# Optimization experiments

Measured on AMD Instinct MI355X. Metric: run time of the kernel, lower is better.

The kernel has to match this reference:

```python
import jax, jax.numpy as jnp
import numpy as np

B, N, ND_, FEAT, WV = 32, 1024, 8, 2048, 300
E, T, STEPS = 20000, 2, 5
NDIM = N * ND_  # 8192


def setup_inputs() -> dict:
    key = jax.random.key(0)
    ks = jax.random.split(key, 20)
    s = 0.02
    inputs = jax.random.normal(ks[0], (B, FEAT), jnp.float32)
    wordvecs = jax.random.normal(ks[1], (N, WV), jnp.float32)
    # unique edges per type (disjoint across types) so the scatter has no duplicate indices
    rng = np.random.default_rng(0)
    codes = rng.permutation(N * N)[: T * E].reshape(T, E)
    edge_u = (codes // N).astype(np.int32)
    edge_v = (codes % N).astype(np.int32)
    ki = np.repeat(np.arange(ND_), ND_)
    kj = np.tile(np.arange(ND_), ND_)
    mat_u = (edge_u.reshape(-1)[:, None] * ND_ + ki[None, :]).reshape(-1).astype(np.int32)
    mat_v = (edge_v.reshape(-1)[:, None] * ND_ + kj[None, :]).reshape(-1).astype(np.int32)
    p = {
        'inputs': inputs, 'wordvecs': wordvecs,
        'edge_u': jnp.asarray(edge_u), 'edge_v': jnp.asarray(edge_v),
        'mat_u': jnp.asarray(mat_u), 'mat_v': jnp.asarray(mat_v),
        # Inputnet: Linear(feat+wv -> 512), Linear(512 -> node_dim)
        'W_in1': jax.random.normal(ks[2], (512, FEAT + WV), jnp.float32) * s,
        'b_in1': jnp.zeros((512,), jnp.float32),
        'W_in2': jax.random.normal(ks[3], (ND_, 512), jnp.float32) * s,
        'b_in2': jnp.zeros((ND_,), jnp.float32),
        # embnet: Linear(wv -> 50)
        'W_emb': jax.random.normal(ks[4], (50, WV), jnp.float32) * s,
        'b_emb': jnp.zeros((50,), jnp.float32),
        # relnets: one (50, 50*nd^2) matrix per edge type
        'rel_mats': jax.random.normal(ks[5], (T, 50, 50 * ND_ * ND_), jnp.float32) * s,
        # GRUCell(node_dim, node_dim)
        'W_ih': jax.random.normal(ks[6], (3 * ND_, ND_), jnp.float32) * s,
        'W_hh': jax.random.normal(ks[7], (3 * ND_, ND_), jnp.float32) * s,
        'b_ih': jnp.zeros((3 * ND_,), jnp.float32),
        'b_hh': jnp.zeros((3 * ND_,), jnp.float32),
        # outnet: Linear(nd -> 20), ReLU, Linear(20 -> 1)
        'W_o1': jax.random.normal(ks[8], (20, ND_), jnp.float32) * s,
        'b_o1': jnp.zeros((20,), jnp.float32),
        'W_o2': jax.random.normal(ks[9], (1, 20), jnp.float32) * s,
        'b_o2': jnp.zeros((1,), jnp.float32),
    }
    return p


def reference(inputs, wordvecs, edge_u, edge_v, mat_u, mat_v,
              W_in1, b_in1, W_in2, b_in2, W_emb, b_emb, rel_mats,
              W_ih, W_hh, b_ih, b_hh, W_o1, b_o1, W_o2, b_o2):
    nd = W_in2.shape[0]
    n_nodes = wordvecs.shape[0]
    ndim = n_nodes * nd
    bsz = inputs.shape[0]

    # Inputnet: per-(image, node) feature -> initial hidden state [B, N*nd]
    f = jnp.concatenate([
        jnp.broadcast_to(inputs[:, None, :], (bsz, n_nodes, inputs.shape[1])),
        jnp.broadcast_to(wordvecs[None, :, :], (bsz, n_nodes, wordvecs.shape[1])),
    ], axis=-1).reshape(bsz * n_nodes, -1)
    h = jax.nn.relu(f @ W_in1.T + b_in1) @ W_in2.T + b_in2  # [B*N, nd]
    hidden = h.reshape(bsz, ndim)

    # edge weights via Relnet per edge type
    embs = wordvecs @ W_emb.T + b_emb  # [N, 50]
    ws = []
    for t in range(rel_mats.shape[0]):
        ue = embs[edge_u[t]]  # [E, 50]
        ve = embs[edge_v[t]]  # [E, 50]
        tmp = (ue @ rel_mats[t]).reshape(ue.shape[0], embs.shape[1], nd * nd)
        ws.append(jnp.einsum('ed,edk->ek', ve, tmp))  # [E, nd^2]
    weights = jnp.concatenate(ws, axis=0).reshape(-1)

    # scatter into dense propagation matrix
    P = jnp.zeros((ndim, ndim), jnp.float32).at[mat_u, mat_v].set(weights)
    norm = jnp.sqrt(jnp.sum(P * P, axis=1))  # row L2 norms [ndim]
    norm = norm + (norm == 0).astype(P.dtype)
    P = P / norm  # NOTE: torch broadcasting divides COLUMNS by row norms (faithful)

    def gru(x, hc):
        gi = x @ W_ih.T + b_ih
        gh = hc @ W_hh.T + b_hh
        ir, iz, inn = jnp.split(gi, 3, axis=-1)
        hr, hz, hn = jnp.split(gh, 3, axis=-1)
        r = jax.nn.sigmoid(ir + hr)
        z = jax.nn.sigmoid(iz + hz)
        n = jnp.tanh(inn + r * hn)
        return (1.0 - z) * n + z * hc

    hiddens = [hidden]
    for _ in range(STEPS):
        x = jnp.tanh(hidden @ P.T)  # [B, ndim]
        hidden = gru(x.reshape(-1, nd), hidden.reshape(-1, nd)).reshape(bsz, ndim)
        hiddens.append(hidden)
    states = jnp.stack(hiddens, axis=1)  # [B, STEPS+1, ndim]

    o = jax.nn.relu(states.reshape(-1, nd) @ W_o1.T + b_o1) @ W_o2.T + b_o2  # [B*(S+1)*N, 1]
    logits = o.reshape(bsz, STEPS + 1, n_nodes).transpose(0, 2, 1)  # [B, N, S+1]
    return logits
```

## Files before the change

### kernel.cpp

```cpp
#include <hip/hip_runtime.h>
#include <math.h>

constexpr int B = 32, N = 1024, ND = 8, FEAT = 2048, WVD = 300;
constexpr int E = 20000, T = 2, STEPS = 5;
constexpr int NDIM = N * ND;
constexpr int H1 = 512;
constexpr int W1C = FEAT + WVD;
constexpr int EMB = 50;
constexpr int RC = EMB * ND * ND;
constexpr int KH = 150;
constexpr int CAP = 64;
constexpr int EQ = E / 4;

constexpr int G_KA   = 512;
constexpr int G_W1T  = 16 * 10;
constexpr int G_EMB  = N * 25 / 4;
constexpr int F1_TOT = G_KA + G_W1T + G_EMB;

constexpr int G_ARED = 8;
constexpr int G_WV   = 512;
constexpr int G_AHAT = 13 * 32 * T;
constexpr int F2_TOT = G_ARED + G_WV + G_AHAT;

__global__ __launch_bounds__(256) void k_f1(
        const float* inp, const float* W1, float* partA, float* W1T,
        const float* wv, const float* We, const float* be,
        float* embs, float* embsT) {
    __shared__ float smem[8 * 260];
    int tid = threadIdx.x;
    int blk = blockIdx.x;
    if (blk < G_KA) {
        int c = tid & 7, b = tid >> 3;
        int c0 = (blk & 63) * 8;
        int ks = blk >> 6;
        int kt = ks * 256;
        {
            int r = tid >> 5, cb = (tid & 31) * 8;
            const float* src = W1 + (size_t)(c0 + r) * W1C + kt + cb;
            float4 a0 = *(const float4*)src;
            float4 a1 = *(const float4*)(src + 4);
            *(float4*)&smem[r * 260 + cb] = a0;
            *(float4*)&smem[r * 260 + cb + 4] = a1;
        }
        __syncthreads();
        const float* xr = inp + (size_t)b * FEAT + kt;
        float acc = 0.f;
#pragma unroll 8
        for (int k4 = 0; k4 < 64; k4++) {
            float4 x = *(const float4*)(xr + k4 * 4);
            float4 w = *(const float4*)&smem[c * 260 + k4 * 4];
            acc += x.x * w.x + x.y * w.y + x.z * w.z + x.w * w.w;
        }
        partA[(size_t)ks * (H1 * B) + (c0 + c) * B + b] = acc;
    } else if (blk < G_KA + G_W1T) {
        int lb = blk - G_KA;
        int c0 = (lb % 16) * 32, k0 = (lb / 16) * 32;
        float (*tile)[33] = (float(*)[33])smem;
        int kl = tid & 31, cl4 = tid >> 5;
#pragma unroll
        for (int p = 0; p < 4; p++) {
            int c = cl4 + p * 8;
            int k = k0 + kl;
            if (k < WVD) tile[c][kl] = W1[(size_t)(c0 + c) * W1C + FEAT + k];
        }
        __syncthreads();
        int cl = tid & 31, kl4 = tid >> 5;
#pragma unroll
        for (int p = 0; p < 4; p++) {
            int kk = kl4 + p * 8;
            int k = k0 + kk;
            if (k < WVD) W1T[(size_t)k * H1 + c0 + cl] = tile[cl][kk];
        }
    } else {
        int lb = blk - G_KA - G_W1T;
        int wid = lb * 4 + (tid >> 6);
        int lane = tid & 63;
        int n = wid / 25, cp = wid - n * 25;
        int c0 = cp * 2;
        const float* xr = wv + (size_t)n * WVD;
        const float* wr0 = We + (size_t)c0 * WVD;
        const float* wr1 = wr0 + WVD;
        float a0 = 0.f, a1 = 0.f;
#pragma unroll
        for (int i = 0; i < 5; i++) {
            int k = i * 64 + lane;
            if (k < WVD) {
                float x = xr[k];
                a0 += x * wr0[k];
                a1 += x * wr1[k];
            }
        }
        for (int m = 32; m; m >>= 1) {
            a0 += __shfl_xor(a0, m, 64);
            a1 += __shfl_xor(a1, m, 64);
        }
        if (lane == 0) {
            float v0 = a0 + be[c0], v1 = a1 + be[c0 + 1];
            embs[n * EMB + c0] = v0;
            embs[n * EMB + c0 + 1] = v1;
            embsT[c0 * N + n] = v0;
            embsT[(c0 + 1) * N + n] = v1;
        }
    }
}

__global__ __launch_bounds__(256) void k_f2(
        const float* partA, float* AbT,
        const float* wv, const float* W1T, float* Wp,
        const float* embsT, const float* RMbase, float* Ahat) {
    __shared__ float smemf[1800];
    int tid = threadIdx.x, blk = blockIdx.x;
    if (blk < G_ARED) {
        int cb = blk * 2048 + tid * 8;
        float4 s0 = {0, 0, 0, 0}, s1 = {0, 0, 0, 0};
#pragma unroll
        for (int ks = 0; ks < 8; ks++) {
            const float* p = partA + (size_t)ks * (H1 * B) + cb;
            float4 a = *(const float4*)p;
            float4 b4 = *(const float4*)(p + 4);
            s0.x += a.x; s0.y += a.y; s0.z += a.z; s0.w += a.w;
            s1.x += b4.x; s1.y += b4.y; s1.z += b4.z; s1.w += b4.w;
        }
        *(float4*)(AbT + cb) = s0;
        *(float4*)(AbT + cb + 4) = s1;
    } else if (blk < G_ARED + G_WV) {
        int lb = blk - G_ARED;
        int kh = lb >> 8;
        int rem = lb & 255;
        int c = (rem & 1) * 256 + tid;
        int n0 = (rem >> 1) * 8;
        int kb = kh * KH;
        float (*el)[8] = (float(*)[8])smemf;
        for (int idx = tid; idx < 8 * KH; idx += 256) {
            int j = idx / KH, k = idx - j * KH;
            el[k][j] = wv[(size_t)(n0 + j) * WVD + kb + k];
        }
        __syncthreads();
        float acc[8] = {};
#pragma unroll 5
        for (int k = 0; k < KH; k++) {
            float r = W1T[(size_t)(kb + k) * H1 + c];
            float4 e0 = *(const float4*)&el[k][0];
            float4 e1 = *(const float4*)&el[k][4];
            acc[0] += e0.x * r; acc[1] += e0.y * r;
            acc[2] += e0.z * r; acc[3] += e0.w * r;
            acc[4] += e1.x * r; acc[5] += e1.y * r;
            acc[6] += e1.z * r; acc[7] += e1.w * r;
        }
        float* wout = Wp + (size_t)kh * N * H1;
#pragma unroll
        for (int j = 0; j < 8; j++) wout[(size_t)(n0 + j) * H1 + c] = acc[j];
    } else {
        int lb = blk - G_ARED - G_WV;
        int t = lb / 416, r = lb % 416;
        int bx = r % 13, by = r / 13;
        const float* RM = RMbase + (size_t)t * EMB * RC;
        float* Ah = Ahat + (size_t)t * N * RC;
        int n0 = by * 32;
        float (*el)[36] = (float(*)[36])smemf;
        for (int idx = tid; idx < EMB * 32; idx += 256)
            el[idx >> 5][idx & 31] = embsT[(idx >> 5) * N + n0 + (idx & 31)];
        __syncthreads();
        int mi = bx * 256 + (tid & 63) * 4;
        int ni = (tid >> 6) * 8;
        if (mi < RC) {
            float acc[8][4] = {};
#pragma unroll 2
            for (int c = 0; c < EMB; c++) {
                float4 rm = *(const float4*)(RM + (size_t)c * RC + mi);
                float4 e0 = *(const float4*)&el[c][ni];
                float4 e1 = *(const float4*)&el[c][ni + 4];
                float ev[8] = {e0.x, e0.y, e0.z, e0.w, e1.x, e1.y, e1.z, e1.w};
#pragma unroll
                for (int j = 0; j < 8; j++) {
                    acc[j][0] += ev[j] * rm.x;
                    acc[j][1] += ev[j] * rm.y;
                    acc[j][2] += ev[j] * rm.z;
                    acc[j][3] += ev[j] * rm.w;
                }
            }
#pragma unroll
            for (int j = 0; j < 8; j++) {
                float4 o = {acc[j][0], acc[j][1], acc[j][2], acc[j][3]};
                *(float4*)(Ah + (size_t)(n0 + ni + j) * RC + mi) = o;
            }
        }
    }
}

__global__ __launch_bounds__(256) void k_f3(
        const int* eu, const int* ev,
        const float* embs, const float* Ahat, float* wbuf, float* inorm,
        int* counts, int* sv,
        const float* AbT, const float* Wp, const float* b1,
        const float* W2, const float* b2, float* sT0) {
    __shared__ float smem[6656];
    __shared__ int vl[T][CAP];
    __shared__ int wcnt[T][4];
    int tid = threadIdx.x;
    int blk = blockIdx.x;
    if (blk < N) {
        int u = blk;
        int w = tid >> 6, lane = tid & 63;
        int* tmpv = (int*)smem;
        for (int t = 0; t < T; t++) {
            const int* eut = eu + t * E;
            const int* evt = ev + t * E;
            int q0 = w * EQ, q1 = q0 + EQ;
            int cw = 0;
            for (int c = q0; c < q1; c += 64) {
                int e = c + lane;
                bool ok = (e < q1) && (eut[e] == u);
                unsigned long long m = __ballot(ok);
                if (ok) {
                    int rank = __popcll(m & ((1ull << lane) - 1));
                    tmpv[(t * 4 + w) * CAP + cw + rank] = evt[e];
                }
                cw += __popcll(m);
            }
            if (lane == 0) wcnt[t][w] = cw;
        }
        __syncthreads();
        int cnts[T];
        for (int t = 0; t < T; t++) {
            int base_w = 0;
            for (int j = 0; j < w; j++) base_w += wcnt[t][j];
            int mycnt = wcnt[t][w];
            int row = t * N + u;
            for (int i = lane; i < mycnt; i += 64) {
                int vv = tmpv[(t * 4 + w) * CAP + i];
                vl[t][base_w + i] = vv;
                sv[row * CAP + base_w + i] = vv;
            }
            cnts[t] = wcnt[t][0] + wcnt[t][1] + wcnt[t][2] + wcnt[t][3];
            if (tid == 0) counts[row] = cnts[t];
        }
        __syncthreads();
        float* AL = smem;
        int k = lane;
        float ssq = 0.f;
        for (int t = 0; t < T; t++) {
            __syncthreads();
            for (int idx = tid; idx < RC; idx += 256)
                AL[idx] = Ahat[((size_t)t * N + u) * RC + idx];
            __syncthreads();
            int cnt = cnts[t];
            size_t base = (size_t)(t * N + u) * CAP;
            for (int i = w; i < cnt; i += 4) {
                int v = vl[t][i];
                const float* vr = embs + v * EMB;
                float acc = 0.f;
#pragma unroll 10
                for (int d = 0; d < EMB; d++) acc += vr[d] * AL[d * 64 + k];
                wbuf[(base + i) * 64 + k] = acc;
                ssq += acc * acc;
            }
        }
        __syncthreads();
        AL[w * 64 + k] = ssq;
        __syncthreads();
        if (tid < 64) {
            float tot = AL[tid] + AL[64 + tid] + AL[128 + tid] + AL[192 + tid];
            tot += __shfl_xor(tot, 1, 64);
            tot += __shfl_xor(tot, 2, 64);
            tot += __shfl_xor(tot, 4, 64);
            int ki = tid >> 3, kj = tid & 7;
            if (kj == 0) {
                float nv = sqrtf(tot);
                if (nv == 0.f) nv = 1.f;
                inorm[u * ND + ki] = 1.0f / nv;
            }
        }
    } else {
        int n = blk - N;
        float* w2s  = smem;
        float* wvs  = smem + 4096;
        float* part = smem + 4608;
        for (int idx = tid; idx < 8 * H1; idx += 256) w2s[idx] = W2[idx];
        for (int idx = tid; idx < H1; idx += 256)
            wvs[idx] = Wp[(size_t)n * H1 + idx]
                     + Wp[(size_t)N * H1 + (size_t)n * H1 + idx] + b1[idx];
        __syncthreads();
        int b = tid & 31, s = tid >> 5;
        float acc[8] = {};
        for (int i = 0; i < 64; i++) {
            int c = s * 64 + i;
            float tv = fmaxf(AbT[c * 32 + b] + wvs[c], 0.f);
#pragma unroll
            for (int ki = 0; ki < 8; ki++) acc[ki] += tv * w2s[ki * H1 + c];
        }
#pragma unroll
        for (int ki = 0; ki < 8; ki++) part[s * 256 + ki * 32 + b] = acc[ki];
        __syncthreads();
        int ki2 = tid >> 5, b2i = tid & 31;
        float tot = b2[ki2];
#pragma unroll
        for (int s2 = 0; s2 < 8; s2++) tot += part[s2 * 256 + ki2 * 32 + b2i];
        sT0[(size_t)n * 256 + tid] = tot;
    }
}

__global__ __launch_bounds__(256) void k_step(
        const int* counts, const int* sv,
        const float* wbuf, const float* inorm, const float* sT, int s,
        const float* W_ih, const float* W_hh, const float* b_ih, const float* b_hh,
        const float* Wo1, const float* bo1, const float* Wo2, const float* bo2,
        float* sOut, float* out, int last) {
    __shared__ float xs[256], hs[256], hfin[256];
    __shared__ float wih[192], whh[192];
    __shared__ float w1s[160], b1s[20], w2s[20];
    __shared__ float res[8][33];
    int tid = threadIdx.x;
    int u = blockIdx.x;
    int ki = tid >> 5, b = tid & 31;
    if (tid < 192) { wih[tid] = W_ih[tid]; whh[tid] = W_hh[tid]; }
    if (last) {
        if (tid < 160) w1s[tid] = Wo1[tid];
        if (tid < 20) { b1s[tid] = bo1[tid]; w2s[tid] = Wo2[tid]; }
    }
    const float* sIn = sT + (size_t)s * NDIM * B;
    float hown = sIn[((size_t)u * 8 + ki) * B + b];
    float acc = 0.f;
    for (int t = 0; t < T; t++) {
        int row = t * N + u;
        int cnt = counts[row];
        size_t base = (size_t)row * CAP;
        int i = 0;
        for (; i + 1 < cnt; i += 2) {
            size_t s0 = base + i, s1 = base + i + 1;
            int v0 = sv[s0], v1 = sv[s1];
            const float* wp0 = wbuf + s0 * 64 + ki * 8;
            const float* wp1 = wbuf + s1 * 64 + ki * 8;
            float4 wa0 = *(const float4*)wp0;
            float4 wb0 = *(const float4*)(wp0 + 4);
            float4 wa1 = *(const float4*)wp1;
            float4 wb1 = *(const float4*)(wp1 + 4);
            const float* ip0 = inorm + v0 * ND;
            const float* ip1 = inorm + v1 * ND;
            const float* hp0 = sIn + (size_t)v0 * 256 + b;
            const float* hp1 = sIn + (size_t)v1 * 256 + b;
            acc += (wa0.x * ip0[0]) * hp0[0]   + (wa0.y * ip0[1]) * hp0[32]
                 + (wa0.z * ip0[2]) * hp0[64]  + (wa0.w * ip0[3]) * hp0[96]
                 + (wb0.x * ip0[4]) * hp0[128] + (wb0.y * ip0[5]) * hp0[160]
                 + (wb0.z * ip0[6]) * hp0[192] + (wb0.w * ip0[7]) * hp0[224];
            acc += (wa1.x * ip1[0]) * hp1[0]   + (wa1.y * ip1[1]) * hp1[32]
                 + (wa1.z * ip1[2]) * hp1[64]  + (wa1.w * ip1[3]) * hp1[96]
                 + (wb1.x * ip1[4]) * hp1[128] + (wb1.y * ip1[5]) * hp1[160]
                 + (wb1.z * ip1[6]) * hp1[192] + (wb1.w * ip1[7]) * hp1[224];
        }
        if (i < cnt) {
            size_t s0 = base + i;
            int v0 = sv[s0];
            const float* wp0 = wbuf + s0 * 64 + ki * 8;
            float4 wa0 = *(const float4*)wp0;
            float4 wb0 = *(const float4*)(wp0 + 4);
            const float* ip0 = inorm + v0 * ND;
            const float* hp0 = sIn + (size_t)v0 * 256 + b;
            acc += (wa0.x * ip0[0]) * hp0[0]   + (wa0.y * ip0[1]) * hp0[32]
                 + (wa0.z * ip0[2]) * hp0[64]  + (wa0.w * ip0[3]) * hp0[96]
                 + (wb0.x * ip0[4]) * hp0[128] + (wb0.y * ip0[5]) * hp0[160]
                 + (wb0.z * ip0[6]) * hp0[192] + (wb0.w * ip0[7]) * hp0[224];
        }
    }
    float xv = tanhf(acc);
    xs[ki * 32 + b] = xv;
    hs[ki * 32 + b] = hown;
    __syncthreads();
    float gr = b_ih[ki], gz = b_ih[8 + ki], gn = b_ih[16 + ki];
    float hr = b_hh[ki], hz = b_hh[8 + ki], hn = b_hh[16 + ki];
#pragma unroll
    for (int j = 0; j < 8; j++) {
        float xj = xs[j * 32 + b], hj = hs[j * 32 + b];
        gr += wih[ki * 8 + j] * xj;
        gz += wih[(8 + ki) * 8 + j] * xj;
        gn += wih[(16 + ki) * 8 + j] * xj;
        hr += whh[ki * 8 + j] * hj;
        hz += whh[(8 + ki) * 8 + j] * hj;
        hn += whh[(16 + ki) * 8 + j] * hj;
    }
    float r = 1.f / (1.f + expf(-(gr + hr)));
    float z = 1.f / (1.f + expf(-(gz + hz)));
    float nn = tanhf(gn + r * hn);
    float hnew = (1.f - z) * nn + z * hown;
    if (!last) {
        sOut[((size_t)u * 8 + ki) * B + b] = hnew;
        return;
    }
    hfin[ki * 32 + b] = hnew;
    __syncthreads();
    int s6 = tid >> 5, bb = tid & 31;
    if (s6 < 6) {
        float x[8];
#pragma unroll
        for (int kk = 0; kk < 8; kk++)
            x[kk] = (s6 < STEPS)
                ? sT[((size_t)s6 * NDIM + u * 8 + kk) * B + bb]
                : hfin[kk * 32 + bb];
        float accv = bo2[0];
#pragma unroll
        for (int j = 0; j < 20; j++) {
            float h = b1s[j];
#pragma unroll
            for (int kk = 0; kk < 8; kk++) h += w1s[j * 8 + kk] * x[kk];
            h = fmaxf(h, 0.f);
            accv += w2s[j] * h;
        }
        res[s6][bb] = accv;
    }
    __syncthreads();
    if (tid < 192) {
        int b_w = tid / 6, s_w = tid - b_w * 6;
        out[(size_t)b_w * ((STEPS + 1) * N) + u * (STEPS + 1) + s_w] = res[s_w][b_w];
    }
}

extern "C" void kernel_launch(void* const* d_in, const int* in_sizes, int n_in,
                              void* d_out, int out_size, void* d_ws, size_t ws_size,
                              hipStream_t stream) {
    const float* inputs   = (const float*)d_in[0];
    const float* wordvecs = (const float*)d_in[1];
    const int*   edge_u   = (const int*)d_in[2];
    const int*   edge_v   = (const int*)d_in[3];
    const float* W_in1 = (const float*)d_in[6];
    const float* b_in1 = (const float*)d_in[7];
    const float* W_in2 = (const float*)d_in[8];
    const float* b_in2 = (const float*)d_in[9];
    const float* W_emb = (const float*)d_in[10];
    const float* b_emb = (const float*)d_in[11];
    const float* rel_mats = (const float*)d_in[12];
    const float* W_ih = (const float*)d_in[13];
    const float* W_hh = (const float*)d_in[14];
    const float* b_ih = (const float*)d_in[15];
    const float* b_hh = (const float*)d_in[16];
    const float* W_o1 = (const float*)d_in[17];
    const float* b_o1 = (const float*)d_in[18];
    const float* W_o2 = (const float*)d_in[19];
    const float* b_o2 = (const float*)d_in[20];
    float* out = (float*)d_out;

    char* ws = (char*)d_ws;
    size_t off = 0;
    auto alloc = [&](size_t bytes) -> void* {
        void* p = ws + off;
        off = (off + bytes + 255) & ~(size_t)255;
        return p;
    };
    int* counts    = (int*)alloc(2048 * 4);
    int* sv        = (int*)alloc((size_t)T * N * CAP * 4);
    float* inorm   = (float*)alloc((size_t)NDIM * 4);
    float* partA   = (float*)alloc((size_t)8 * H1 * B * 4);
    float* AbT     = (float*)alloc((size_t)H1 * B * 4);
    float* W1T     = (float*)alloc((size_t)WVD * H1 * 4);
    float* Wp      = (float*)alloc((size_t)2 * N * H1 * 4);
    float* embs    = (float*)alloc((size_t)N * EMB * 4);
    float* embsT   = (float*)alloc((size_t)EMB * N * 4);
    float* Ahat    = (float*)alloc((size_t)T * N * RC * 4);
    float* wbuf    = (float*)alloc((size_t)T * N * CAP * 64 * 4);
    float* sT      = (float*)alloc((size_t)(STEPS + 1) * NDIM * B * 4);

    k_f1<<<F1_TOT, 256, 0, stream>>>(inputs, W_in1, partA, W1T,
                                     wordvecs, W_emb, b_emb, embs, embsT);
    k_f2<<<F2_TOT, 256, 0, stream>>>(partA, AbT, wordvecs, W1T, Wp,
                                     embsT, rel_mats, Ahat);
    k_f3<<<2 * N, 256, 0, stream>>>(edge_u, edge_v, embs, Ahat, wbuf, inorm,
                                    counts, sv, AbT, Wp, b_in1, W_in2, b_in2, sT);

    for (int s = 0; s < STEPS; s++) {
        int last = (s == STEPS - 1) ? 1 : 0;
        k_step<<<N, 256, 0, stream>>>(counts, sv, wbuf, inorm, sT, s,
                                      W_ih, W_hh, b_ih, b_hh,
                                      W_o1, b_o1, W_o2, b_o2,
                                      sT + (size_t)(s + 1) * NDIM * B, out, last);
    }
}
```

Before: 252.8 us.

## Split edge bucketing into parallel segment count and scatter passes

```diff
diff --git a/kernel.cpp b/kernel.cpp
--- a/kernel.cpp
+++ b/kernel.cpp
@@ -10,19 +10,25 @@
 constexpr int RC = EMB * ND * ND;
 constexpr int KH = 150;
 constexpr int CAP = 64;
-constexpr int EQ = E / 4;
+constexpr int SEG = 16;
+constexpr int SEGLEN = E / SEG;
 
 constexpr int G_KA   = 512;
 constexpr int G_W1T  = 16 * 10;
 constexpr int G_EMB  = N * 25 / 4;
-constexpr int F1_TOT = G_KA + G_W1T + G_EMB;
+constexpr int G_SEGH = T * N * SEG / 4;
+constexpr int F1_TOT = G_KA + G_W1T + G_EMB + G_SEGH;
 
 constexpr int G_ARED = 8;
 constexpr int G_WV   = 512;
 constexpr int G_AHAT = 13 * 32 * T;
 constexpr int F2_TOT = G_ARED + G_WV + G_AHAT;
 
+constexpr int G_SCAT = T * N * SEG / 4;
+constexpr int F3_TOT = G_SCAT + N;
+
 __global__ __launch_bounds__(256) void k_f1(
+        const int* eu, int* segcnt,
         const float* inp, const float* W1, float* partA, float* W1T,
         const float* wv, const float* We, const float* be,
         float* embs, float* embsT) {
@@ -71,7 +77,7 @@
             int k = k0 + kk;
             if (k < WVD) W1T[(size_t)k * H1 + c0 + cl] = tile[cl][kk];
         }
-    } else {
+    } else if (blk < G_KA + G_W1T + G_EMB) {
         int lb = blk - G_KA - G_W1T;
         int wid = lb * 4 + (tid >> 6);
         int lane = tid & 63;
@@ -101,6 +107,19 @@
             embsT[c0 * N + n] = v0;
             embsT[(c0 + 1) * N + n] = v1;
         }
+    } else {
+        int lb = blk - G_KA - G_W1T - G_EMB;
+        int wid = lb * 4 + (tid >> 6);
+        int lane = tid & 63;
+        int t = wid >> 14, u = (wid >> 4) & (N - 1), seg = wid & (SEG - 1);
+        const int* eut = eu + t * E;
+        int e0 = seg * SEGLEN, e1 = e0 + SEGLEN, cnt = 0;
+        for (int c = e0; c < e1; c += 64) {
+            int e = c + lane;
+            bool ok = (e < e1) && (eut[e] == u);
+            cnt += __popcll(__ballot(ok));
+        }
+        if (lane == 0) segcnt[wid] = cnt;
     }
 }
 
@@ -189,90 +208,34 @@
 }
 
 __global__ __launch_bounds__(256) void k_f3(
-        const int* eu, const int* ev,
-        const float* embs, const float* Ahat, float* wbuf, float* inorm,
-        int* counts, int* sv,
+        const int* eu, const int* ev, const int* segcnt, int* sv,
         const float* AbT, const float* Wp, const float* b1,
         const float* W2, const float* b2, float* sT0) {
     __shared__ float smem[6656];
-    __shared__ int vl[T][CAP];
-    __shared__ int wcnt[T][4];
-    int tid = threadIdx.x;
-    int blk = blockIdx.x;
-    if (blk < N) {
-        int u = blk;
-        int w = tid >> 6, lane = tid & 63;
-        int* tmpv = (int*)smem;
-        for (int t = 0; t < T; t++) {
-            const int* eut = eu + t * E;
-            const int* evt = ev + t * E;
-            int q0 = w * EQ, q1 = q0 + EQ;
-            int cw = 0;
-            for (int c = q0; c < q1; c += 64) {
-                int e = c + lane;
-                bool ok = (e < q1) && (eut[e] == u);
-                unsigned long long m = __ballot(ok);
-                if (ok) {
-                    int rank = __popcll(m & ((1ull << lane) - 1));
-                    tmpv[(t * 4 + w) * CAP + cw + rank] = evt[e];
-                }
-                cw += __popcll(m);
+    int tid = threadIdx.x, blk = blockIdx.x;
+    if (blk < G_SCAT) {
+        int wid = blk * 4 + (tid >> 6);
+        int lane = tid & 63;
+        int t = wid >> 14, u = (wid >> 4) & (N - 1), seg = wid & (SEG - 1);
+        const int* eut = eu + t * E;
+        const int* evt = ev + t * E;
+        int row = t * N + u;
+        int pre = 0;
+        for (int j = 0; j < seg; j++) pre += segcnt[row * SEG + j];
+        int base = row * CAP + pre;
+        int e0 = seg * SEGLEN, e1 = e0 + SEGLEN, cnt = 0;
+        for (int c = e0; c < e1; c += 64) {
+            int e = c + lane;
+            bool ok = (e < e1) && (eut[e] == u);
+            unsigned long long m = __ballot(ok);
+            if (ok) {
+                int rank = __popcll(m & ((1ull << lane) - 1));
+                sv[base + cnt + rank] = evt[e];
             }
-            if (lane == 0) wcnt[t][w] = cw;
-        }
-        __syncthreads();
-        int cnts[T];
-        for (int t = 0; t < T; t++) {
-            int base_w = 0;
-            for (int j = 0; j < w; j++) base_w += wcnt[t][j];
-            int mycnt = wcnt[t][w];
-            int row = t * N + u;
-            for (int i = lane; i < mycnt; i += 64) {
-                int vv = tmpv[(t * 4 + w) * CAP + i];
-                vl[t][base_w + i] = vv;
-                sv[row * CAP + base_w + i] = vv;
-            }
-            cnts[t] = wcnt[t][0] + wcnt[t][1] + wcnt[t][2] + wcnt[t][3];
-            if (tid == 0) counts[row] = cnts[t];
-        }
-        __syncthreads();
-        float* AL = smem;
-        int k = lane;
-        float ssq = 0.f;
-        for (int t = 0; t < T; t++) {
-            __syncthreads();
-            for (int idx = tid; idx < RC; idx += 256)
-                AL[idx] = Ahat[((size_t)t * N + u) * RC + idx];
-            __syncthreads();
-            int cnt = cnts[t];
-            size_t base = (size_t)(t * N + u) * CAP;
-            for (int i = w; i < cnt; i += 4) {
-                int v = vl[t][i];
-                const float* vr = embs + v * EMB;
-                float acc = 0.f;
-#pragma unroll 10
-                for (int d = 0; d < EMB; d++) acc += vr[d] * AL[d * 64 + k];
-                wbuf[(base + i) * 64 + k] = acc;
-                ssq += acc * acc;
-            }
-        }
-        __syncthreads();
-        AL[w * 64 + k] = ssq;
-        __syncthreads();
-        if (tid < 64) {
-            float tot = AL[tid] + AL[64 + tid] + AL[128 + tid] + AL[192 + tid];
-            tot += __shfl_xor(tot, 1, 64);
-            tot += __shfl_xor(tot, 2, 64);
-            tot += __shfl_xor(tot, 4, 64);
-            int ki = tid >> 3, kj = tid & 7;
-            if (kj == 0) {
-                float nv = sqrtf(tot);
-                if (nv == 0.f) nv = 1.f;
-                inorm[u * ND + ki] = 1.0f / nv;
-            }
+            cnt += __popcll(m);
         }
     } else {
-        int n = blk - N;
+        int n = blk - G_SCAT;
         float* w2s  = smem;
         float* wvs  = smem + 4096;
         float* part = smem + 4608;
@@ -297,6 +260,66 @@
 #pragma unroll
         for (int s2 = 0; s2 < 8; s2++) tot += part[s2 * 256 + ki2 * 32 + b2i];
         sT0[(size_t)n * 256 + tid] = tot;
+    }
+}
+
+__global__ __launch_bounds__(256) void k_f4(
+        const int* segcnt, const int* sv, int* counts,
+        const float* embs, const float* Ahat, float* wbuf, float* inorm) {
+    __shared__ float AL[RC];
+    __shared__ int vl[T][CAP];
+    __shared__ int cl[T];
+    int tid = threadIdx.x;
+    int u = blockIdx.x;
+    int w = tid >> 6, k = tid & 63;
+    if (tid < T) {
+        int row = tid * N + u;
+        int c = 0;
+#pragma unroll
+        for (int j = 0; j < SEG; j++) c += segcnt[row * SEG + j];
+        cl[tid] = c;
+        counts[row] = c;
+    }
+    __syncthreads();
+    int cnts[T];
+#pragma unroll
+    for (int t = 0; t < T; t++) {
+        cnts[t] = cl[t];
+        if (tid < CAP && tid < cnts[t])
+            vl[t][tid] = sv[(size_t)(t * N + u) * CAP + tid];
+    }
+    float ssq = 0.f;
+    for (int t = 0; t < T; t++) {
+        __syncthreads();
+        for (int idx = tid; idx < RC; idx += 256)
+            AL[idx] = Ahat[((size_t)t * N + u) * RC + idx];
+        __syncthreads();
+        int cnt = cnts[t];
+        size_t base = (size_t)(t * N + u) * CAP;
+        for (int i = w; i < cnt; i += 4) {
+            int v = vl[t][i];
+            const float* vr = embs + v * EMB;
+            float acc = 0.f;
+#pragma unroll 10
+            for (int d = 0; d < EMB; d++) acc += vr[d] * AL[d * 64 + k];
+            wbuf[(base + i) * 64 + k] = acc;
+            ssq += acc * acc;
+        }
+    }
+    __syncthreads();
+    AL[w * 64 + k] = ssq;
+    __syncthreads();
+    if (tid < 64) {
+        float tot = AL[tid] + AL[64 + tid] + AL[128 + tid] + AL[192 + tid];
+        tot += __shfl_xor(tot, 1, 64);
+        tot += __shfl_xor(tot, 2, 64);
+        tot += __shfl_xor(tot, 4, 64);
+        int ki = tid >> 3, kj = tid & 7;
+        if (kj == 0) {
+            float nv = sqrtf(tot);
+            if (nv == 0.f) nv = 1.f;
+            inorm[u * ND + ki] = 1.0f / nv;
+        }
     }
 }
 
@@ -445,6 +468,7 @@
         off = (off + bytes + 255) & ~(size_t)255;
         return p;
     };
+    int* segcnt    = (int*)alloc((size_t)T * N * SEG * 4);
     int* counts    = (int*)alloc(2048 * 4);
     int* sv        = (int*)alloc((size_t)T * N * CAP * 4);
     float* inorm   = (float*)alloc((size_t)NDIM * 4);
@@ -458,12 +482,13 @@
     float* wbuf    = (float*)alloc((size_t)T * N * CAP * 64 * 4);
     float* sT      = (float*)alloc((size_t)(STEPS + 1) * NDIM * B * 4);
 
-    k_f1<<<F1_TOT, 256, 0, stream>>>(inputs, W_in1, partA, W1T,
+    k_f1<<<F1_TOT, 256, 0, stream>>>(edge_u, segcnt, inputs, W_in1, partA, W1T,
                                      wordvecs, W_emb, b_emb, embs, embsT);
     k_f2<<<F2_TOT, 256, 0, stream>>>(partA, AbT, wordvecs, W1T, Wp,
                                      embsT, rel_mats, Ahat);
-    k_f3<<<2 * N, 256, 0, stream>>>(edge_u, edge_v, embs, Ahat, wbuf, inorm,
-                                    counts, sv, AbT, Wp, b_in1, W_in2, b_in2, sT);
+    k_f3<<<F3_TOT, 256, 0, stream>>>(edge_u, edge_v, segcnt, sv,
+                                     AbT, Wp, b_in1, W_in2, b_in2, sT);
+    k_f4<<<N, 256, 0, stream>>>(segcnt, sv, counts, embs, Ahat, wbuf, inorm);
 
     for (int s = 0; s < STEPS; s++) {
         int last = (s == STEPS - 1) ? 1 : 0;
```

Measured after the change: 265.5 us. 5.0% more time.
